# Kernel optimization log

Measured on AMD Instinct MI355X. Metric: run time of the kernel, lower is better.

The kernel has to match this reference:

```python
import jax, jax.numpy as jnp
import numpy as np


def setup_inputs() -> dict:
    key = jax.random.key(0)
    kx, ks = jax.random.split(key)
    M, N, D = 8192, 8192, 512
    X = jax.random.normal(kx, (M, D), dtype=jnp.float32)
    svs = jax.random.normal(ks, (N, D), dtype=jnp.float32)
    # scale = 1/(2*sigma^2); a plausible fitted value for standard-normal data
    scale = jnp.asarray(0.01, dtype=jnp.float32)
    return {"X": X, "svs": svs, "scale": scale}


def reference(X, svs, scale):
    N, D = svs.shape
    x2 = jnp.sum(X * X, axis=-1, keepdims=True)          # [M, 1]
    s2 = jnp.sum(svs * svs, axis=-1)                      # [N]
    dist2 = x2 + s2[None, :] - 2.0 * (X @ svs.T)          # [M, N]
    dist2 = jnp.maximum(dist2, 0.0)
    log_p = (jax.scipy.special.logsumexp(-scale * dist2, axis=-1)
             - jnp.log(jnp.asarray(N, dtype=X.dtype))
             + (D / 2) * jnp.log(scale / jnp.pi))
    return log_p
```

## Files before the change

### kernel.cpp

```cpp
#include <hip/hip_runtime.h>
#include <hip/hip_bf16.h>
#include <math.h>

typedef __attribute__((ext_vector_type(8))) short short8;
typedef __attribute__((ext_vector_type(4))) float f32x4;

#define BM 128
#define BN 128
#define BK 64

__global__ __launch_bounds__(256) void prep_kernel(
    const float* __restrict__ X, const float* __restrict__ S,
    __hip_bfloat16* __restrict__ Xb, __hip_bfloat16* __restrict__ Sb,
    float* __restrict__ x2, float* __restrict__ s2,
    float* __restrict__ rowsum, int M, int R, int Dv)
{
    const int gid  = blockIdx.x * 256 + threadIdx.x;
    const int nthr = gridDim.x * 256;

    for (int i = gid; i < M; i += nthr) rowsum[i] = 0.f;

    const int lane = threadIdx.x & 63;
    const int wid  = gid >> 6;
    const int nw   = nthr >> 6;

    for (int row = wid; row < R; row += nw) {
        const float* rp;
        __hip_bfloat16* op;
        float* sq;
        if (row < M) { rp = X + (size_t)row * Dv;       op = Xb + (size_t)row * Dv;       sq = x2 + row; }
        else         { rp = S + (size_t)(row - M) * Dv; op = Sb + (size_t)(row - M) * Dv; sq = s2 + (row - M); }

        float acc = 0.f;
        for (int k = lane * 8; k < Dv; k += 64 * 8) {
            float4 v0 = *(const float4*)(rp + k);
            float4 v1 = *(const float4*)(rp + k + 4);
            acc += v0.x * v0.x + v0.y * v0.y + v0.z * v0.z + v0.w * v0.w;
            acc += v1.x * v1.x + v1.y * v1.y + v1.z * v1.z + v1.w * v1.w;
            union { __hip_bfloat16 h[8]; uint4 u; } pk;
            pk.h[0] = __float2bfloat16(v0.x);
            pk.h[1] = __float2bfloat16(v0.y);
            pk.h[2] = __float2bfloat16(v0.z);
            pk.h[3] = __float2bfloat16(v0.w);
            pk.h[4] = __float2bfloat16(v1.x);
            pk.h[5] = __float2bfloat16(v1.y);
            pk.h[6] = __float2bfloat16(v1.z);
            pk.h[7] = __float2bfloat16(v1.w);
            *(uint4*)(op + k) = pk.u;
        }
#pragma unroll
        for (int off = 1; off < 64; off <<= 1)
            acc += __shfl_xor(acc, off, 64);
        if (lane == 0) *sq = acc;
    }
}

template<int DVC>
__global__ __launch_bounds__(256, 4) void kde_gemm_kernel(
    const __hip_bfloat16* __restrict__ Xb,
    const __hip_bfloat16* __restrict__ Sb,
    const float* __restrict__ x2,
    const float* __restrict__ s2,
    const float* __restrict__ scale_p,
    float* __restrict__ rowsum,
    int M, int N, int Dv)
{
    const int D = DVC ? DVC : Dv;

    __shared__ char smem[32768];
    __hip_bfloat16* As = (__hip_bfloat16*)smem;
    __hip_bfloat16* Bs = (__hip_bfloat16*)(smem + 16384);

    const int tid  = threadIdx.x;
    const int wave = tid >> 6;
    const int lane = tid & 63;
    const int quad = lane >> 4;
    const int l16  = lane & 15;

    const int m0 = blockIdx.x * BM;
    const int n0 = blockIdx.y * BN;
    const int wm = (wave & 1) * 64;
    const int wn = (wave >> 1) * 64;

    const float sc = *scale_p;

    f32x4 acc[4][4] = {};

    const int srow0 = wave * 8 + (lane >> 3);
    const int cg    = (lane & 7) ^ (lane >> 3);
    const __hip_bfloat16* gA = Xb + (size_t)(m0 + srow0) * D + cg * 8;
    const __hip_bfloat16* gB = Sb + (size_t)(n0 + srow0) * D + cg * 8;

#pragma unroll
    for (int k0 = 0; k0 < D; k0 += BK) {
        __syncthreads();
#pragma unroll
        for (int rd = 0; rd < 4; ++rd)
            __builtin_amdgcn_global_load_lds(
                (const __attribute__((address_space(1))) void*)(gA + (size_t)rd * 32 * D + k0),
                (__attribute__((address_space(3))) void*)(smem + rd * 4096 + wave * 1024),
                16, 0, 0);
#pragma unroll
        for (int rd = 0; rd < 4; ++rd)
            __builtin_amdgcn_global_load_lds(
                (const __attribute__((address_space(1))) void*)(gB + (size_t)rd * 32 * D + k0),
                (__attribute__((address_space(3))) void*)(smem + 16384 + rd * 4096 + wave * 1024),
                16, 0, 0);
        __syncthreads();

#pragma unroll
        for (int ks = 0; ks < 2; ++ks) {
            short8 a_frag[4], b_frag[4];
            const int cph = ((ks * 4 + quad) ^ (l16 & 7)) * 8;
#pragma unroll
            for (int mi = 0; mi < 4; ++mi)
                a_frag[mi] = *(const short8*)(As + (wm + mi * 16 + l16) * BK + cph);
#pragma unroll
            for (int ni = 0; ni < 4; ++ni)
                b_frag[ni] = *(const short8*)(Bs + (wn + ni * 16 + l16) * BK + cph);
#pragma unroll
            for (int mi = 0; mi < 4; ++mi)
#pragma unroll
                for (int ni = 0; ni < 4; ++ni)
                    acc[mi][ni] = __builtin_amdgcn_mfma_f32_16x16x32_bf16(
                        a_frag[mi], b_frag[ni], acc[mi][ni], 0, 0, 0);
        }
    }

    __syncthreads();
    float* wred = (float*)smem + wave * (64 * 20);

    float s2v[4];
#pragma unroll
    for (int ni = 0; ni < 4; ++ni)
        s2v[ni] = s2[n0 + wn + ni * 16 + l16];

#pragma unroll
    for (int mi = 0; mi < 4; ++mi) {
#pragma unroll
        for (int r = 0; r < 4; ++r) {
            const int rowL = mi * 16 + quad * 4 + r;
            const float xv = x2[m0 + wm + rowL];
            float sum = 0.f;
#pragma unroll
            for (int ni = 0; ni < 4; ++ni) {
                float d2 = xv + s2v[ni] - 2.0f * acc[mi][ni][r];
                d2 = fmaxf(d2, 0.f);
                sum += __expf(-sc * d2);
            }
            wred[rowL * 20 + l16] = sum;
        }
    }
    __syncthreads();

    float4 p0 = *(float4*)(wred + lane * 20 + 0);
    float4 p1 = *(float4*)(wred + lane * 20 + 4);
    float4 p2 = *(float4*)(wred + lane * 20 + 8);
    float4 p3 = *(float4*)(wred + lane * 20 + 12);
    float s = (p0.x + p0.y + p0.z + p0.w) + (p1.x + p1.y + p1.z + p1.w)
            + (p2.x + p2.y + p2.z + p2.w) + (p3.x + p3.y + p3.z + p3.w);
    atomicAdd(&rowsum[m0 + wm + lane], s);
}

__global__ void finalize_kernel(const float* __restrict__ rowsum,
                                const float* __restrict__ scale_p,
                                float* __restrict__ out, int M, int N, int Dv) {
    const int m = blockIdx.x * 256 + threadIdx.x;
    if (m < M) {
        const float sc = *scale_p;
        const float cst = -logf((float)N) + 0.5f * (float)Dv * logf(sc / 3.14159265358979f);
        out[m] = logf(rowsum[m]) + cst;
    }
}

extern "C" void kernel_launch(void* const* d_in, const int* in_sizes, int n_in,
                              void* d_out, int out_size, void* d_ws, size_t ws_size,
                              hipStream_t stream) {
    const float* X       = (const float*)d_in[0];
    const float* S       = (const float*)d_in[1];
    const float* scale_p = (const float*)d_in[2];
    float* out = (float*)d_out;

    const int M  = out_size;
    const int Dv = in_sizes[0] / M;
    const int N  = in_sizes[1] / Dv;

    char* ws = (char*)d_ws;
    __hip_bfloat16* Xb = (__hip_bfloat16*)ws;
    __hip_bfloat16* Sb = (__hip_bfloat16*)(ws + (size_t)M * Dv * 2);
    float* x2     = (float*)(ws + (size_t)M * Dv * 2 + (size_t)N * Dv * 2);
    float* s2     = x2 + M;
    float* rowsum = s2 + N;

    prep_kernel<<<512, 256, 0, stream>>>(X, S, Xb, Sb, x2, s2, rowsum, M, M + N, Dv);

    dim3 grid(M / BM, N / BN);
    if (Dv == 512)
        kde_gemm_kernel<512><<<grid, 256, 0, stream>>>(Xb, Sb, x2, s2, scale_p, rowsum, M, N, Dv);
    else
        kde_gemm_kernel<0><<<grid, 256, 0, stream>>>(Xb, Sb, x2, s2, scale_p, rowsum, M, N, Dv);

    finalize_kernel<<<(M + 255) / 256, 256, 0, stream>>>(rowsum, scale_p, out, M, N, Dv);
}
```

Measured before the change: 145.8 us.

## Switch GEMM operands from bf16 to fp8 e4m3 with scaled MFMA

```diff
diff --git a/kernel.cpp b/kernel.cpp
--- a/kernel.cpp
+++ b/kernel.cpp
@@ -1,17 +1,19 @@
 #include <hip/hip_runtime.h>
 #include <hip/hip_bf16.h>
+#include <hip/hip_fp8.h>
 #include <math.h>
 
-typedef __attribute__((ext_vector_type(8))) short short8;
+typedef __attribute__((ext_vector_type(4))) int   int4v;
+typedef __attribute__((ext_vector_type(8))) int   int8v;
 typedef __attribute__((ext_vector_type(4))) float f32x4;
 
 #define BM 128
 #define BN 128
-#define BK 64
+#define BK 128
 
 __global__ __launch_bounds__(256) void prep_kernel(
     const float* __restrict__ X, const float* __restrict__ S,
-    __hip_bfloat16* __restrict__ Xb, __hip_bfloat16* __restrict__ Sb,
+    unsigned char* __restrict__ Xq, unsigned char* __restrict__ Sq,
     float* __restrict__ x2, float* __restrict__ s2,
     float* __restrict__ rowsum, int M, int R, int Dv)
 {
@@ -26,10 +28,10 @@
 
     for (int row = wid; row < R; row += nw) {
         const float* rp;
-        __hip_bfloat16* op;
+        unsigned char* op;
         float* sq;
-        if (row < M) { rp = X + (size_t)row * Dv;       op = Xb + (size_t)row * Dv;       sq = x2 + row; }
-        else         { rp = S + (size_t)(row - M) * Dv; op = Sb + (size_t)(row - M) * Dv; sq = s2 + (row - M); }
+        if (row < M) { rp = X + (size_t)row * Dv;       op = Xq + (size_t)row * Dv;       sq = x2 + row; }
+        else         { rp = S + (size_t)(row - M) * Dv; op = Sq + (size_t)(row - M) * Dv; sq = s2 + (row - M); }
 
         float acc = 0.f;
         for (int k = lane * 8; k < Dv; k += 64 * 8) {
@@ -37,16 +39,16 @@
             float4 v1 = *(const float4*)(rp + k + 4);
             acc += v0.x * v0.x + v0.y * v0.y + v0.z * v0.z + v0.w * v0.w;
             acc += v1.x * v1.x + v1.y * v1.y + v1.z * v1.z + v1.w * v1.w;
-            union { __hip_bfloat16 h[8]; uint4 u; } pk;
-            pk.h[0] = __float2bfloat16(v0.x);
-            pk.h[1] = __float2bfloat16(v0.y);
-            pk.h[2] = __float2bfloat16(v0.z);
-            pk.h[3] = __float2bfloat16(v0.w);
-            pk.h[4] = __float2bfloat16(v1.x);
-            pk.h[5] = __float2bfloat16(v1.y);
-            pk.h[6] = __float2bfloat16(v1.z);
-            pk.h[7] = __float2bfloat16(v1.w);
-            *(uint4*)(op + k) = pk.u;
+            union { __hip_fp8_e4m3 h[8]; uint2 u; } pk;
+            pk.h[0] = __hip_fp8_e4m3(v0.x);
+            pk.h[1] = __hip_fp8_e4m3(v0.y);
+            pk.h[2] = __hip_fp8_e4m3(v0.z);
+            pk.h[3] = __hip_fp8_e4m3(v0.w);
+            pk.h[4] = __hip_fp8_e4m3(v1.x);
+            pk.h[5] = __hip_fp8_e4m3(v1.y);
+            pk.h[6] = __hip_fp8_e4m3(v1.z);
+            pk.h[7] = __hip_fp8_e4m3(v1.w);
+            *(uint2*)(op + k) = pk.u;
         }
 #pragma unroll
         for (int off = 1; off < 64; off <<= 1)
@@ -56,9 +58,9 @@
 }
 
 template<int DVC>
-__global__ __launch_bounds__(256, 4) void kde_gemm_kernel(
-    const __hip_bfloat16* __restrict__ Xb,
-    const __hip_bfloat16* __restrict__ Sb,
+__global__ __launch_bounds__(256, 3) void kde_gemm_kernel(
+    const unsigned char* __restrict__ Xq,
+    const unsigned char* __restrict__ Sq,
     const float* __restrict__ x2,
     const float* __restrict__ s2,
     const float* __restrict__ scale_p,
@@ -68,8 +70,8 @@
     const int D = DVC ? DVC : Dv;
 
     __shared__ char smem[32768];
-    __hip_bfloat16* As = (__hip_bfloat16*)smem;
-    __hip_bfloat16* Bs = (__hip_bfloat16*)(smem + 16384);
+    unsigned char* As = (unsigned char*)smem;
+    unsigned char* Bs = (unsigned char*)(smem + 16384);
 
     const int tid  = threadIdx.x;
     const int wave = tid >> 6;
@@ -88,8 +90,8 @@
 
     const int srow0 = wave * 8 + (lane >> 3);
     const int cg    = (lane & 7) ^ (lane >> 3);
-    const __hip_bfloat16* gA = Xb + (size_t)(m0 + srow0) * D + cg * 8;
-    const __hip_bfloat16* gB = Sb + (size_t)(n0 + srow0) * D + cg * 8;
+    const unsigned char* gA = Xq + (size_t)(m0 + srow0) * D + cg * 16;
+    const unsigned char* gB = Sq + (size_t)(n0 + srow0) * D + cg * 16;
 
 #pragma unroll
     for (int k0 = 0; k0 < D; k0 += BK) {
@@ -108,23 +110,31 @@
                 16, 0, 0);
         __syncthreads();
 
-#pragma unroll
-        for (int ks = 0; ks < 2; ++ks) {
-            short8 a_frag[4], b_frag[4];
-            const int cph = ((ks * 4 + quad) ^ (l16 & 7)) * 8;
-#pragma unroll
-            for (int mi = 0; mi < 4; ++mi)
-                a_frag[mi] = *(const short8*)(As + (wm + mi * 16 + l16) * BK + cph);
+        const int e = l16 & 7;
+        int8v a_frag[4], b_frag[4];
+#pragma unroll
+        for (int mi = 0; mi < 4; ++mi) {
+            const unsigned char* rowp = As + (wm + mi * 16 + l16) * 128;
+            int4v lo = *(const int4v*)(rowp + ((2 * quad)     ^ e) * 16);
+            int4v hi = *(const int4v*)(rowp + ((2 * quad + 1) ^ e) * 16);
+            a_frag[mi] = (int8v){lo.x, lo.y, lo.z, lo.w, hi.x, hi.y, hi.z, hi.w};
+        }
+#pragma unroll
+        for (int ni = 0; ni < 4; ++ni) {
+            const unsigned char* rowp = Bs + (wn + ni * 16 + l16) * 128;
+            int4v lo = *(const int4v*)(rowp + ((2 * quad)     ^ e) * 16);
+            int4v hi = *(const int4v*)(rowp + ((2 * quad + 1) ^ e) * 16);
+            b_frag[ni] = (int8v){lo.x, lo.y, lo.z, lo.w, hi.x, hi.y, hi.z, hi.w};
+        }
+#pragma unroll
+        for (int mi = 0; mi < 4; ++mi)
 #pragma unroll
             for (int ni = 0; ni < 4; ++ni)
-                b_frag[ni] = *(const short8*)(Bs + (wn + ni * 16 + l16) * BK + cph);
-#pragma unroll
-            for (int mi = 0; mi < 4; ++mi)
-#pragma unroll
-                for (int ni = 0; ni < 4; ++ni)
-                    acc[mi][ni] = __builtin_amdgcn_mfma_f32_16x16x32_bf16(
-                        a_frag[mi], b_frag[ni], acc[mi][ni], 0, 0, 0);
-        }
+                acc[mi][ni] = __builtin_amdgcn_mfma_scale_f32_16x16x128_f8f6f4(
+                    a_frag[mi], b_frag[ni], acc[mi][ni],
+                    0, 0,
+                    0, 0x7F7F7F7F,
+                    0, 0x7F7F7F7F);
     }
 
     __syncthreads();
@@ -186,19 +196,19 @@
     const int N  = in_sizes[1] / Dv;
 
     char* ws = (char*)d_ws;
-    __hip_bfloat16* Xb = (__hip_bfloat16*)ws;
-    __hip_bfloat16* Sb = (__hip_bfloat16*)(ws + (size_t)M * Dv * 2);
-    float* x2     = (float*)(ws + (size_t)M * Dv * 2 + (size_t)N * Dv * 2);
+    unsigned char* Xq = (unsigned char*)ws;
+    unsigned char* Sq = (unsigned char*)(ws + (size_t)M * Dv);
+    float* x2     = (float*)(ws + (size_t)M * Dv + (size_t)N * Dv);
     float* s2     = x2 + M;
     float* rowsum = s2 + N;
 
-    prep_kernel<<<512, 256, 0, stream>>>(X, S, Xb, Sb, x2, s2, rowsum, M, M + N, Dv);
+    prep_kernel<<<512, 256, 0, stream>>>(X, S, Xq, Sq, x2, s2, rowsum, M, M + N, Dv);
 
     dim3 grid(M / BM, N / BN);
     if (Dv == 512)
-        kde_gemm_kernel<512><<<grid, 256, 0, stream>>>(Xb, Sb, x2, s2, scale_p, rowsum, M, N, Dv);
+        kde_gemm_kernel<512><<<grid, 256, 0, stream>>>(Xq, Sq, x2, s2, scale_p, rowsum, M, N, Dv);
     else
-        kde_gemm_kernel<0><<<grid, 256, 0, stream>>>(Xb, Sb, x2, s2, scale_p, rowsum, M, N, Dv);
+        kde_gemm_kernel<0><<<grid, 256, 0, stream>>>(Xq, Sq, x2, s2, scale_p, rowsum, M, N, Dv);
 
     finalize_kernel<<<(M + 255) / 256, 256, 0, stream>>>(rowsum, scale_p, out, M, N, Dv);
 }
```

Measured after the change: 122.1 us. 1.19x faster.
